# Optimization experiments

Measured on AMD Instinct MI355X. Metric: run time of the kernel, lower is better.

The kernel has to match this reference:

```python
import jax, jax.numpy as jnp
import numpy as np

SEQ_LEN = 2048
N_FFT = 4096   # rfft length n >= seq_len (repo uses next power of two of ~2*seq)
K = 24         # num_eigh
D = 768        # n_embd
BATCH = 1


def _spectral_filters(seq_len: int, k: int) -> jnp.ndarray:
    # Hankel matrix Z[i,j] = 2 / ((i+j)^3 - (i+j)), 1-indexed
    e = np.arange(1, seq_len + 1, dtype=np.float64)
    ipj = e[:, None] + e[None, :]
    Z = 2.0 / (ipj ** 3 - ipj)
    sigma, phi = np.linalg.eigh(Z)
    sigma, phi = sigma[-k:], phi[:, -k:]
    phi = phi * sigma ** 0.25
    return jnp.asarray(phi, dtype=jnp.float32)  # (seq_len, K)


def setup_inputs() -> dict:
    key = jax.random.key(0)
    k1, k2, k3 = jax.random.split(key, 3)
    x = jax.random.normal(k1, (BATCH, SEQ_LEN, D), dtype=jnp.float32)
    M_phi_plus = jax.random.normal(k2, (K, D, D), dtype=jnp.float32) * 0.02
    M_phi_minus = jax.random.normal(k3, (K, D, D), dtype=jnp.float32) * 0.02
    phi = _spectral_filters(SEQ_LEN, K)
    return {"x": x, "phi": phi, "M_phi_plus": M_phi_plus, "M_phi_minus": M_phi_minus}


def _convolve(u, v, n):
    # u: (b, seq, d), v: (seq, K)
    bsz, seq, d = u.shape
    k = v.shape[1]
    # alternating sign sequence (+1, -1, +1, ...)
    sgn = jnp.where(jnp.arange(seq) % 2 == 1, -1.0, 1.0)[None, :, None, None]  # (1,seq,1,1)
    V = jnp.fft.rfft(v.reshape(1, seq, k, 1, 1).astype(jnp.float32), n=n, axis=1)
    u4 = jnp.broadcast_to(u[:, :, None, :], (bsz, seq, k, d))  # (b,seq,K,d)
    U = jnp.stack([u4, u4 * sgn], axis=-1).astype(jnp.float32)  # (b,seq,K,d,2)
    Uf = jnp.fft.rfft(U, n=n, axis=1)
    U_conv = jnp.fft.irfft(V * Uf, n=n, axis=1)[:, :seq]  # (b,seq,K,d,2)
    U_plus = U_conv[..., 0]
    U_minus = U_conv[..., 1] * sgn
    return U_plus, U_minus


def reference(x, phi, M_phi_plus, M_phi_minus):
    U_plus, U_minus = _convolve(x, phi, N_FFT)
    spectral_plus = jnp.einsum('bskd,kde->bse', U_plus, M_phi_plus)
    spectral_minus = jnp.einsum('bskd,kde->bse', U_minus, M_phi_minus)
    return spectral_plus + spectral_minus
```

## Files before the change

kernel.cpp:

```cpp
#include <hip/hip_runtime.h>
#include <hip/hip_bf16.h>
#include <stdint.h>

#define SEQ 2048
#define DDIM 768
#define KF 24
#define NKV 48
#define NZC 8

typedef unsigned short ushort_t;
typedef __attribute__((ext_vector_type(8))) short short8;
typedef __attribute__((ext_vector_type(4))) float f32x4;

typedef __attribute__((address_space(3))) uint32_t lds_u32;
typedef __attribute__((address_space(1))) uint32_t glb_u32;

__device__ __forceinline__ unsigned short f2bf(float f) {
    union { float f; uint32_t u; } v; v.f = f;
    uint32_t u = v.u;
    return (unsigned short)((u + 0x7fff + ((u >> 16) & 1)) >> 16);
}


__global__ void k_pack_x(const float* __restrict__ x, ushort_t* __restrict__ xpk) {
    int b = blockIdx.x;
    int tt = b / 12, ks = b % 12;
    int tid = threadIdx.x;
    ushort_t* dst = xpk + (size_t)b * 8192;
    const float* src = x + (size_t)tt * 128 * DDIM + ks * 64;
#pragma unroll
    for (int p = 0; p < 4; ++p) {
        int s = p * 256 + tid;
        int row = s >> 3, sl = s & 7;
        const float* rp = src + (size_t)row * DDIM + sl * 8;
        float4 a = *(const float4*)rp;
        float4 c = *(const float4*)(rp + 4);
        ushort_t v[8] = {f2bf(a.x), f2bf(a.y), f2bf(a.z), f2bf(a.w),
                         f2bf(c.x), f2bf(c.y), f2bf(c.z), f2bf(c.w)};
        *(uint4*)(dst + row * 64 + ((sl ^ (row & 7)) << 3)) = *(uint4*)v;
    }
}

__global__ void k_pack_M(const float* __restrict__ Mp, const float* __restrict__ Mm,
                         ushort_t* __restrict__ Mpk) {
    __shared__ ushort_t lt[128 * 66];
    int b = blockIdx.x;
    int kv = b / 72; int rem = b % 72; int et = rem / 12, ks = rem % 12;
    const float* src = ((kv < KF) ? Mp + (size_t)kv * DDIM * DDIM
                                  : Mm + (size_t)(kv - KF) * DDIM * DDIM)
                       + (size_t)(ks * 64) * DDIM + et * 128;
    int tid = threadIdx.x;
#pragma unroll
    for (int p = 0; p < 32; ++p) {
        int lin = p * 256 + tid;
        int d = lin >> 7, e = lin & 127;
        lt[e * 66 + d] = f2bf(src[(size_t)d * DDIM + e]);
    }
    __syncthreads();
    ushort_t* dst = Mpk + (size_t)b * 8192;
#pragma unroll
    for (int p = 0; p < 4; ++p) {
        int s = p * 256 + tid; int row = s >> 3, sl = s & 7;
        ushort_t v[8];
#pragma unroll
        for (int j = 0; j < 8; ++j) v[j] = lt[row * 66 + sl * 8 + j];
        *(uint4*)(dst + row * 64 + ((sl ^ (row & 7)) << 3)) = *(uint4*)v;
    }
}

__global__ void k_build_T(const float* __restrict__ phi, ushort_t* __restrict__ Tpk) {
    __shared__ float phiL[256];
    int b = blockIdx.x;
    int kv = b >> 4, dm = b & 15;
    int k = kv % KF; bool neg = kv >= KF;
    int tid = threadIdx.x;
    int tau = 128 * dm - 127 + tid;
    float v = 0.f;
    if (tid < 255 && tau >= 0 && tau < SEQ) {
        v = phi[(size_t)tau * KF + k];
        if (neg && (tau & 1)) v = -v;
    }
    phiL[tid] = v;
    __syncthreads();
    ushort_t* dst = Tpk + (size_t)b * 2 * 8192;
#pragma unroll
    for (int h = 0; h < 2; ++h) {
#pragma unroll
        for (int p = 0; p < 4; ++p) {
            int s = p * 256 + tid; int row = s >> 3, sl = s & 7;
            ushort_t v8[8];
#pragma unroll
            for (int j = 0; j < 8; ++j) {
                int col = h * 64 + sl * 8 + j;
                v8[j] = f2bf(phiL[row - col + 127]);
            }
            *(uint4*)(dst + h * 8192 + row * 64 + ((sl ^ (row & 7)) << 3)) = *(uint4*)v8;
        }
    }
}


__device__ __forceinline__ void stage_img(const ushort_t* __restrict__ src,
                                          ushort_t* lds, int tid) {
    int wave = tid >> 6, lane = tid & 63;
    const char* s = (const char*)src + wave * 1024 + lane * 16;
    char* l = (char*)lds + wave * 1024;
#pragma unroll
    for (int p = 0; p < 4; ++p) {
        __builtin_amdgcn_global_load_lds((const glb_u32*)(s + p * 4096),
                                         (lds_u32*)(l + p * 4096), 16, 0, 0);
    }
}

__device__ __forceinline__ void mfma_img(const ushort_t* As, const ushort_t* Bs,
                                         int lane, int wm, int wn, f32x4 acc[4][4]) {
#pragma unroll
    for (int kk = 0; kk < 2; ++kk) {
        int slot = kk * 4 + (lane >> 4);
        short8 av[4], bv[4];
#pragma unroll
        for (int m = 0; m < 4; ++m) {
            int row = wm * 64 + m * 16 + (lane & 15);
            av[m] = *(const short8*)(As + row * 64 + ((slot ^ (row & 7)) << 3));
        }
#pragma unroll
        for (int n = 0; n < 4; ++n) {
            int row = wn * 64 + n * 16 + (lane & 15);
            bv[n] = *(const short8*)(Bs + row * 64 + ((slot ^ (row & 7)) << 3));
        }
#pragma unroll
        for (int m = 0; m < 4; ++m)
#pragma unroll
            for (int n = 0; n < 4; ++n)
                acc[m][n] = __builtin_amdgcn_mfma_f32_16x16x32_bf16(av[m], bv[n], acc[m][n], 0, 0, 0);
    }
}

__global__ __launch_bounds__(256, 3)
void k_gemm_A(const ushort_t* __restrict__ Mpk, const ushort_t* __restrict__ xpk,
              ushort_t* __restrict__ Apk, int kvLo) {
    __shared__ ushort_t smem[16384];
    ushort_t* As = smem; ushort_t* Bs = smem + 8192;
    int bid = blockIdx.x;
    int kvi = bid / 96; int rem = bid % 96; int et = rem / 16, tt = rem % 16;
    int kv = kvLo + kvi;
    const ushort_t* Asrc = Mpk + ((size_t)(kv * 6 + et) * 12) * 8192;
    const ushort_t* Bsrc = xpk + (size_t)(tt * 12) * 8192;
    int tid = threadIdx.x, lane = tid & 63, wave = tid >> 6;
    int wm = wave >> 1, wn = wave & 1;

    f32x4 acc[4][4];
#pragma unroll
    for (int m = 0; m < 4; ++m)
#pragma unroll
        for (int n = 0; n < 4; ++n) acc[m][n] = (f32x4){0.f, 0.f, 0.f, 0.f};

    for (int ks = 0; ks < 12; ++ks) {
        __syncthreads();
        stage_img(Asrc + ks * 8192, As, tid);
        stage_img(Bsrc + ks * 8192, Bs, tid);
        __syncthreads();
        mfma_img(As, Bs, lane, wm, wn, acc);
    }

    __syncthreads();
#pragma unroll
    for (int m = 0; m < 4; ++m) {
        int rb = wm * 64 + m * 16 + ((lane >> 4) << 2);
#pragma unroll
        for (int n = 0; n < 4; ++n) {
            int cb = wn * 64 + n * 16 + (lane & 15);
            int h = cb >> 6, c6 = cb & 63, sl = c6 >> 3, j = c6 & 7;
#pragma unroll
            for (int r = 0; r < 4; ++r) {
                int row = rb + r;
                smem[h * 8192 + row * 64 + ((sl ^ (row & 7)) << 3) + j] = f2bf(acc[m][n][r]);
            }
        }
    }
    __syncthreads();
    uint4* d4 = (uint4*)(Apk + ((size_t)((kvi * 6 + et) * 16 + tt) * 2) * 8192);
    const uint4* s4 = (const uint4*)smem;
#pragma unroll
    for (int p = 0; p < 8; ++p) d4[p * 256 + tid] = s4[p * 256 + tid];
}

__global__ __launch_bounds__(256, 2)
void k_gemm_Bv4(const ushort_t* __restrict__ Tpk, const ushort_t* __restrict__ Apk,
                float* __restrict__ outz, int kvLo, int nkv) {
    __shared__ ushort_t smem[2][2][8192];

    int bid = blockIdx.x;
    int lid = (bid & 7) * 54 + (bid >> 3);
    int et = lid / 72;
    int cidx = lid % 72;
    int i1 = 0, zc = 0, base = 0;
#pragma unroll
    for (int t = 0; t < 16; ++t) {
        int cand = 15 - t;
        int nc = (cand >> 1) + 1;
        if (cidx < base + nc) { i1 = cand; zc = cidx - base; break; }
        base += nc;
    }
    int jlo = zc * 2;
    int jhi = (jlo + 1 < i1) ? (jlo + 1) : i1;
    int NS = nkv * (jhi - jlo + 1) * 2;

    int tid = threadIdx.x, lane = tid & 63, wave = tid >> 6;
    int wm = wave >> 1, wn = wave & 1;

    f32x4 acc[4][4];
#pragma unroll
    for (int m = 0; m < 4; ++m)
#pragma unroll
        for (int n = 0; n < 4; ++n) acc[m][n] = (f32x4){0.f, 0.f, 0.f, 0.f};

    auto timg = [&](int kv, int jj, int h) -> const ushort_t* {
        return Tpk + ((size_t)(((kvLo + kv) * 16 + (i1 - jj)) * 2 + h)) * 8192;
    };
    auto aimg = [&](int kv, int jj, int h) -> const ushort_t* {
        return Apk + ((size_t)(((kv * 6 + et) * 16 + jj) * 2 + h)) * 8192;
    };
    auto stage4 = [&](const ushort_t* src, ushort_t* dst) {
        const char* s = (const char*)src + wave * 4096 + lane * 16;
        char* l = (char*)dst + wave * 4096;
#pragma unroll
        for (int p = 0; p < 4; ++p)
            __builtin_amdgcn_global_load_lds((const glb_u32*)(s + p * 1024),
                                             (lds_u32*)(l + p * 1024), 16, 0, 0);
    };

    int kv = 0, jj = jlo, h = 0;
    stage4(timg(kv, jj, h), smem[0][0]);
    stage4(aimg(kv, jj, h), smem[0][1]);

    for (int s = 0; s < NS; ++s) {
        int c = s & 1;
        int nh = h ^ 1, njj = jj, nkvv = kv;
        if (!nh) { njj = jj + 1; if (njj > jhi) { njj = jlo; nkvv = kv + 1; } }
        bool more = (s + 1 < NS);

        if (more) {
            stage4(timg(nkvv, njj, nh), smem[c ^ 1][0]);
            asm volatile("s_waitcnt vmcnt(4)" ::: "memory");
        } else {
            asm volatile("s_waitcnt vmcnt(0)" ::: "memory");
        }
        __builtin_amdgcn_s_barrier();
        __builtin_amdgcn_sched_barrier(0);

        const ushort_t* As = smem[c][0];
        const ushort_t* Bs = smem[c][1];
        short8 av[2][4], bv[2][4];
#pragma unroll
        for (int kk = 0; kk < 2; ++kk) {
            int slot = kk * 4 + (lane >> 4);
#pragma unroll
            for (int m = 0; m < 4; ++m) {
                int row = wm * 64 + m * 16 + (lane & 15);
                av[kk][m] = *(const short8*)(As + row * 64 + ((slot ^ (row & 7)) << 3));
            }
#pragma unroll
            for (int n = 0; n < 4; ++n) {
                int row = wn * 64 + n * 16 + (lane & 15);
                bv[kk][n] = *(const short8*)(Bs + row * 64 + ((slot ^ (row & 7)) << 3));
            }
        }
        if (more) stage4(aimg(nkvv, njj, nh), smem[c ^ 1][1]);

        asm volatile("s_waitcnt lgkmcnt(0)" ::: "memory");
        __builtin_amdgcn_sched_barrier(0);

        __builtin_amdgcn_s_setprio(1);
#pragma unroll
        for (int kk = 0; kk < 2; ++kk)
#pragma unroll
            for (int m = 0; m < 4; ++m)
#pragma unroll
                for (int n = 0; n < 4; ++n)
                    acc[m][n] = __builtin_amdgcn_mfma_f32_16x16x32_bf16(av[kk][m], bv[kk][n], acc[m][n], 0, 0, 0);
        __builtin_amdgcn_s_setprio(0);
        __builtin_amdgcn_s_barrier();
        kv = nkvv; jj = njj; h = nh;
    }

    float* dst = outz + ((size_t)zc * SEQ + (size_t)i1 * 128) * DDIM + et * 128;
#pragma unroll
    for (int m = 0; m < 4; ++m) {
        int rb = wm * 64 + m * 16 + ((lane >> 4) << 2);
#pragma unroll
        for (int n = 0; n < 4; ++n) {
            int cb = wn * 64 + n * 16 + (lane & 15);
#pragma unroll
            for (int r = 0; r < 4; ++r) {
                float* p = dst + (size_t)(rb + r) * DDIM + cb;
                *p += acc[m][n][r];
            }
        }
    }
}

__global__ void k_reduce(const float* __restrict__ outz, float* __restrict__ out, int n4) {
    int idx = blockIdx.x * blockDim.x + threadIdx.x;
    if (idx < n4) {
        float4 s = ((const float4*)outz)[idx];
#pragma unroll
        for (int z = 1; z < NZC; ++z) {
            float4 t = ((const float4*)(outz + (size_t)z * SEQ * DDIM))[idx];
            s.x += t.x; s.y += t.y; s.z += t.z; s.w += t.w;
        }
        ((float4*)out)[idx] = s;
    }
}

extern "C" void kernel_launch(void* const* d_in, const int* in_sizes, int n_in,
                              void* d_out, int out_size, void* d_ws, size_t ws_size,
                              hipStream_t stream) {
    (void)in_sizes; (void)n_in;
    const float* x   = (const float*)d_in[0];
    const float* phi = (const float*)d_in[1];
    const float* Mp  = (const float*)d_in[2];
    const float* Mm  = (const float*)d_in[3];
    float* out = (float*)d_out;

    char* ws = (char*)d_ws;
    size_t off = 0;
    auto alloc = [&](size_t bytes) { size_t o = off; off += (bytes + 255) & ~(size_t)255; return o; };
    size_t o_xpk  = alloc((size_t)16 * 12 * 8192 * 2);
    size_t o_Mpk  = alloc((size_t)NKV * 6 * 12 * 8192 * 2);
    size_t o_Tpk  = alloc((size_t)NKV * 16 * 2 * 8192 * 2);
    size_t o_outz = alloc((size_t)NZC * SEQ * DDIM * 4);
    size_t fixed = off;

    int C = 0;
    const int cand[4] = {48, 24, 16, 8};
    for (int ci = 0; ci < 4; ++ci) {
        if (fixed + (size_t)cand[ci] * 6 * 16 * 2 * 8192 * 2 <= ws_size) { C = cand[ci]; break; }
    }
    if (C == 0) {
        hipMemsetAsync(d_out, 0, (size_t)out_size * 4, stream);
        return;
    }
    size_t o_Apk = alloc((size_t)C * 6 * 16 * 2 * 8192 * 2);

    ushort_t* xpk = (ushort_t*)(ws + o_xpk);
    ushort_t* Mpk = (ushort_t*)(ws + o_Mpk);
    ushort_t* Tpk = (ushort_t*)(ws + o_Tpk);
    float*    outz = (float*)(ws + o_outz);
    ushort_t* Apk = (ushort_t*)(ws + o_Apk);

    k_pack_x<<<16 * 12, 256, 0, stream>>>(x, xpk);
    k_pack_M<<<NKV * 6 * 12, 256, 0, stream>>>(Mp, Mm, Mpk);
    k_build_T<<<NKV * 16, 256, 0, stream>>>(phi, Tpk);
    hipMemsetAsync(outz, 0, (size_t)NZC * SEQ * DDIM * 4, stream);

    for (int kvLo = 0; kvLo < NKV; kvLo += C) {
        k_gemm_A<<<C * 96, 256, 0, stream>>>(Mpk, xpk, Apk, kvLo);
        k_gemm_Bv4<<<432, 256, 0, stream>>>(Tpk, Apk, outz, kvLo, C);
    }
    int n4 = SEQ * DDIM / 4;
    k_reduce<<<(n4 + 255) / 256, 256, 0, stream>>>(outz, out, n4);
}
```

Measured before the change: 363.1 us.

## Double-buffer k_gemm_A staging, split fragment reads, drop memset and trim reduce

k_gemm_A now double-buffers its LDS tiles with async global-to-LDS loads and prefetches the next K-slice while the current one is computed. Both GEMMs split fragment reads into two halves so the MFMAs on the first half can start before the second half arrives. The outz memset is removed: the first chunk writes its results directly and later chunks accumulate. k_reduce sums only the z-slices that can be nonzero for each row. In exchange, k_gemm_A's launch bound drops from 3 to 2 blocks per CU because of the doubled LDS, and correctness now depends on the first pass writing every outz element the reduce reads.

```diff
diff --git a/kernel.cpp b/kernel.cpp
--- a/kernel.cpp
+++ b/kernel.cpp
@@ -100,70 +100,90 @@
 }
 
 
-__device__ __forceinline__ void stage_img(const ushort_t* __restrict__ src,
-                                          ushort_t* lds, int tid) {
-    int wave = tid >> 6, lane = tid & 63;
-    const char* s = (const char*)src + wave * 1024 + lane * 16;
-    char* l = (char*)lds + wave * 1024;
-#pragma unroll
-    for (int p = 0; p < 4; ++p) {
-        __builtin_amdgcn_global_load_lds((const glb_u32*)(s + p * 4096),
-                                         (lds_u32*)(l + p * 4096), 16, 0, 0);
-    }
-}
-
-__device__ __forceinline__ void mfma_img(const ushort_t* As, const ushort_t* Bs,
-                                         int lane, int wm, int wn, f32x4 acc[4][4]) {
-#pragma unroll
-    for (int kk = 0; kk < 2; ++kk) {
-        int slot = kk * 4 + (lane >> 4);
-        short8 av[4], bv[4];
-#pragma unroll
-        for (int m = 0; m < 4; ++m) {
-            int row = wm * 64 + m * 16 + (lane & 15);
-            av[m] = *(const short8*)(As + row * 64 + ((slot ^ (row & 7)) << 3));
-        }
-#pragma unroll
-        for (int n = 0; n < 4; ++n) {
-            int row = wn * 64 + n * 16 + (lane & 15);
-            bv[n] = *(const short8*)(Bs + row * 64 + ((slot ^ (row & 7)) << 3));
-        }
-#pragma unroll
-        for (int m = 0; m < 4; ++m)
-#pragma unroll
-            for (int n = 0; n < 4; ++n)
-                acc[m][n] = __builtin_amdgcn_mfma_f32_16x16x32_bf16(av[m], bv[n], acc[m][n], 0, 0, 0);
-    }
-}
-
-__global__ __launch_bounds__(256, 3)
+__device__ __forceinline__ void read_frags(const ushort_t* As, const ushort_t* Bs,
+                                           int lane, int wm, int wn, int kk,
+                                           short8 av[4], short8 bv[4]) {
+    int slot = kk * 4 + (lane >> 4);
+#pragma unroll
+    for (int m = 0; m < 4; ++m) {
+        int row = wm * 64 + m * 16 + (lane & 15);
+        av[m] = *(const short8*)(As + row * 64 + ((slot ^ (row & 7)) << 3));
+    }
+#pragma unroll
+    for (int n = 0; n < 4; ++n) {
+        int row = wn * 64 + n * 16 + (lane & 15);
+        bv[n] = *(const short8*)(Bs + row * 64 + ((slot ^ (row & 7)) << 3));
+    }
+}
+
+__device__ __forceinline__ void mfma16(const short8 av[4], const short8 bv[4], f32x4 acc[4][4]) {
+    __builtin_amdgcn_s_setprio(1);
+#pragma unroll
+    for (int m = 0; m < 4; ++m)
+#pragma unroll
+        for (int n = 0; n < 4; ++n)
+            acc[m][n] = __builtin_amdgcn_mfma_f32_16x16x32_bf16(av[m], bv[n], acc[m][n], 0, 0, 0);
+    __builtin_amdgcn_s_setprio(0);
+}
+
+__global__ __launch_bounds__(256, 2)
 void k_gemm_A(const ushort_t* __restrict__ Mpk, const ushort_t* __restrict__ xpk,
               ushort_t* __restrict__ Apk, int kvLo) {
-    __shared__ ushort_t smem[16384];
-    ushort_t* As = smem; ushort_t* Bs = smem + 8192;
+    __shared__ ushort_t smem[2][2][8192];
     int bid = blockIdx.x;
     int kvi = bid / 96; int rem = bid % 96; int et = rem / 16, tt = rem % 16;
     int kv = kvLo + kvi;
-    const ushort_t* Asrc = Mpk + ((size_t)(kv * 6 + et) * 12) * 8192;
-    const ushort_t* Bsrc = xpk + (size_t)(tt * 12) * 8192;
+    const ushort_t* Abase = Mpk + ((size_t)(kv * 6 + et) * 12) * 8192;
+    const ushort_t* Bbase = xpk + (size_t)(tt * 12) * 8192;
     int tid = threadIdx.x, lane = tid & 63, wave = tid >> 6;
     int wm = wave >> 1, wn = wave & 1;
 
+    auto stage4 = [&](const ushort_t* src, ushort_t* dst) {
+        const char* s = (const char*)src + wave * 4096 + lane * 16;
+        char* l = (char*)dst + wave * 4096;
+#pragma unroll
+        for (int p = 0; p < 4; ++p)
+            __builtin_amdgcn_global_load_lds((const glb_u32*)(s + p * 1024),
+                                             (lds_u32*)(l + p * 1024), 16, 0, 0);
+    };
+
     f32x4 acc[4][4];
 #pragma unroll
     for (int m = 0; m < 4; ++m)
 #pragma unroll
         for (int n = 0; n < 4; ++n) acc[m][n] = (f32x4){0.f, 0.f, 0.f, 0.f};
 
-    for (int ks = 0; ks < 12; ++ks) {
-        __syncthreads();
-        stage_img(Asrc + ks * 8192, As, tid);
-        stage_img(Bsrc + ks * 8192, Bs, tid);
-        __syncthreads();
-        mfma_img(As, Bs, lane, wm, wn, acc);
-    }
-
-    __syncthreads();
+    stage4(Abase, smem[0][0]);
+    stage4(Bbase, smem[0][1]);
+
+    for (int s = 0; s < 12; ++s) {
+        int c = s & 1;
+        bool more = (s + 1 < 12);
+        if (more) {
+            stage4(Abase + (s + 1) * 8192, smem[c ^ 1][0]);
+            asm volatile("s_waitcnt vmcnt(4)" ::: "memory");
+        } else {
+            asm volatile("s_waitcnt vmcnt(0)" ::: "memory");
+        }
+        __builtin_amdgcn_s_barrier();
+        __builtin_amdgcn_sched_barrier(0);
+
+        const ushort_t* As = smem[c][0];
+        const ushort_t* Bs = smem[c][1];
+        short8 av0[4], bv0[4], av1[4], bv1[4];
+        read_frags(As, Bs, lane, wm, wn, 0, av0, bv0);
+        asm volatile("s_waitcnt lgkmcnt(0)" ::: "memory");
+        __builtin_amdgcn_sched_barrier(0);
+        read_frags(As, Bs, lane, wm, wn, 1, av1, bv1);
+        if (more) stage4(Bbase + (s + 1) * 8192, smem[c ^ 1][1]);
+        mfma16(av0, bv0, acc);
+        asm volatile("s_waitcnt lgkmcnt(0)" ::: "memory");
+        __builtin_amdgcn_sched_barrier(0);
+        mfma16(av1, bv1, acc);
+        __builtin_amdgcn_s_barrier();
+    }
+
+    ushort_t* sm = &smem[0][0][0];
 #pragma unroll
     for (int m = 0; m < 4; ++m) {
         int rb = wm * 64 + m * 16 + ((lane >> 4) << 2);
@@ -174,20 +194,20 @@
 #pragma unroll
             for (int r = 0; r < 4; ++r) {
                 int row = rb + r;
-                smem[h * 8192 + row * 64 + ((sl ^ (row & 7)) << 3) + j] = f2bf(acc[m][n][r]);
+                sm[h * 8192 + row * 64 + ((sl ^ (row & 7)) << 3) + j] = f2bf(acc[m][n][r]);
             }
         }
     }
     __syncthreads();
     uint4* d4 = (uint4*)(Apk + ((size_t)((kvi * 6 + et) * 16 + tt) * 2) * 8192);
-    const uint4* s4 = (const uint4*)smem;
+    const uint4* s4 = (const uint4*)sm;
 #pragma unroll
     for (int p = 0; p < 8; ++p) d4[p * 256 + tid] = s4[p * 256 + tid];
 }
 
 __global__ __launch_bounds__(256, 2)
-void k_gemm_Bv4(const ushort_t* __restrict__ Tpk, const ushort_t* __restrict__ Apk,
-                float* __restrict__ outz, int kvLo, int nkv) {
+void k_gemm_Bv5(const ushort_t* __restrict__ Tpk, const ushort_t* __restrict__ Apk,
+                float* __restrict__ outz, int kvLo, int nkv, int accum) {
     __shared__ ushort_t smem[2][2][8192];
 
     int bid = blockIdx.x;
@@ -251,35 +271,16 @@
 
         const ushort_t* As = smem[c][0];
         const ushort_t* Bs = smem[c][1];
-        short8 av[2][4], bv[2][4];
-#pragma unroll
-        for (int kk = 0; kk < 2; ++kk) {
-            int slot = kk * 4 + (lane >> 4);
-#pragma unroll
-            for (int m = 0; m < 4; ++m) {
-                int row = wm * 64 + m * 16 + (lane & 15);
-                av[kk][m] = *(const short8*)(As + row * 64 + ((slot ^ (row & 7)) << 3));
-            }
-#pragma unroll
-            for (int n = 0; n < 4; ++n) {
-                int row = wn * 64 + n * 16 + (lane & 15);
-                bv[kk][n] = *(const short8*)(Bs + row * 64 + ((slot ^ (row & 7)) << 3));
-            }
-        }
+        short8 av0[4], bv0[4], av1[4], bv1[4];
+        read_frags(As, Bs, lane, wm, wn, 0, av0, bv0);
+        asm volatile("s_waitcnt lgkmcnt(0)" ::: "memory");
+        __builtin_amdgcn_sched_barrier(0);
+        read_frags(As, Bs, lane, wm, wn, 1, av1, bv1);
         if (more) stage4(aimg(nkvv, njj, nh), smem[c ^ 1][1]);
-
+        mfma16(av0, bv0, acc);
         asm volatile("s_waitcnt lgkmcnt(0)" ::: "memory");
         __builtin_amdgcn_sched_barrier(0);
-
-        __builtin_amdgcn_s_setprio(1);
-#pragma unroll
-        for (int kk = 0; kk < 2; ++kk)
-#pragma unroll
-            for (int m = 0; m < 4; ++m)
-#pragma unroll
-                for (int n = 0; n < 4; ++n)
-                    acc[m][n] = __builtin_amdgcn_mfma_f32_16x16x32_bf16(av[kk][m], bv[kk][n], acc[m][n], 0, 0, 0);
-        __builtin_amdgcn_s_setprio(0);
+        mfma16(av1, bv1, acc);
         __builtin_amdgcn_s_barrier();
         kv = nkvv; jj = njj; h = nh;
     }
@@ -294,7 +295,9 @@
 #pragma unroll
             for (int r = 0; r < 4; ++r) {
                 float* p = dst + (size_t)(rb + r) * DDIM + cb;
-                *p += acc[m][n][r];
+                float v = acc[m][n][r];
+                if (accum) v += *p;
+                *p = v;
             }
         }
     }
@@ -303,9 +306,11 @@
 __global__ void k_reduce(const float* __restrict__ outz, float* __restrict__ out, int n4) {
     int idx = blockIdx.x * blockDim.x + threadIdx.x;
     if (idx < n4) {
+        int srow = idx / (DDIM / 4);
+        int zmax = (srow >> 8);
+        if (zmax > NZC - 1) zmax = NZC - 1;
         float4 s = ((const float4*)outz)[idx];
-#pragma unroll
-        for (int z = 1; z < NZC; ++z) {
+        for (int z = 1; z <= zmax; ++z) {
             float4 t = ((const float4*)(outz + (size_t)z * SEQ * DDIM))[idx];
             s.x += t.x; s.y += t.y; s.z += t.z; s.w += t.w;
         }
@@ -352,11 +357,10 @@
     k_pack_x<<<16 * 12, 256, 0, stream>>>(x, xpk);
     k_pack_M<<<NKV * 6 * 12, 256, 0, stream>>>(Mp, Mm, Mpk);
     k_build_T<<<NKV * 16, 256, 0, stream>>>(phi, Tpk);
-    hipMemsetAsync(outz, 0, (size_t)NZC * SEQ * DDIM * 4, stream);
 
     for (int kvLo = 0; kvLo < NKV; kvLo += C) {
         k_gemm_A<<<C * 96, 256, 0, stream>>>(Mpk, xpk, Apk, kvLo);
-        k_gemm_Bv4<<<432, 256, 0, stream>>>(Tpk, Apk, outz, kvLo, C);
+        k_gemm_Bv5<<<432, 256, 0, stream>>>(Tpk, Apk, outz, kvLo, C, kvLo > 0);
     }
     int n4 = SEQ * DDIM / 4;
     k_reduce<<<(n4 + 255) / 256, 256, 0, stream>>>(outz, out, n4);
```

Result: no change. 360.8 us (-0.6%).
